# Performance work log

Hardware: AMD Instinct MI355X
Metric: run time of the kernel (lower is better)

## Reference

```python
import jax, jax.numpy as jnp
import numpy as np

N_NODES = 70839  # num_user + num_item from config
N_EDGES = 2_000_000
EMB_DIM = 64
EPS = 1e-12  # torch F.normalize default eps


def setup_inputs() -> dict:
    key = jax.random.key(0)
    k1, k2, k3, k4 = jax.random.split(key, 4)
    ego_embedding = jax.random.normal(k1, (N_NODES, EMB_DIM), dtype=jnp.float32)
    edge_weight = jax.random.uniform(k2, (N_EDGES,), dtype=jnp.float32)
    edge_src = jax.random.randint(k3, (N_EDGES,), 0, N_NODES, dtype=jnp.int32)
    edge_dst = jax.random.randint(k4, (N_EDGES,), 0, N_NODES, dtype=jnp.int32)
    return {
        "ego_embedding": ego_embedding,
        "edge_weight": edge_weight,
        "edge_src": edge_src,
        "edge_dst": edge_dst,
    }


def reference(ego_embedding, edge_weight, edge_src, edge_dst):
    # message: m_e = h[src_e] * w_e   (u_mul_e)
    m = ego_embedding[edge_src] * edge_weight[:, None]          # [E, D]
    # reduce: h_v = sum_{e: dst_e = v} m_e   (fn.sum)
    h = jax.ops.segment_sum(m, edge_dst, num_segments=N_NODES)  # [N, D]
    # F.normalize(h, dim=1, p=2): x / max(||x||_2, eps)
    norm = jnp.linalg.norm(h, axis=1, keepdims=True)
    return h / jnp.maximum(norm, EPS)
```

## Files before the change

kernel.cpp:

```cpp
#include <hip/hip_runtime.h>
#include <hip/hip_fp16.h>

#define EMB_D 64
#define SB 1024
#define SPAN 64
#define SPAN_SH 6
#define MAXG 2048
#define NCHUNK2 512
#define CHMAX 4096
#define TILE2 2048
#define CAST_BLOCKS 256


__device__ __forceinline__ float h15_to_float(unsigned int bits) {
    return __half2float(__ushort_as_half((unsigned short)bits));
}

__device__ __forceinline__ uint4 rowld(const char* base, unsigned int pk,
                                       unsigned int qlo) {
    return *reinterpret_cast<const uint4*>(base + ((pk >> 15) * 128u + qlo));
}

__device__ __forceinline__ void fma8(float4& a, float4& b, uint4 r, float wt) {
    float2 x01 = __half22float2(*reinterpret_cast<__half2*>(&r.x));
    float2 x23 = __half22float2(*reinterpret_cast<__half2*>(&r.y));
    float2 x45 = __half22float2(*reinterpret_cast<__half2*>(&r.z));
    float2 x67 = __half22float2(*reinterpret_cast<__half2*>(&r.w));
    a.x = fmaf(x01.x, wt, a.x); a.y = fmaf(x01.y, wt, a.y);
    a.z = fmaf(x23.x, wt, a.z); a.w = fmaf(x23.y, wt, a.w);
    b.x = fmaf(x45.x, wt, b.x); b.y = fmaf(x45.y, wt, b.y);
    b.z = fmaf(x67.x, wt, b.z); b.w = fmaf(x67.y, wt, b.w);
}

__global__ void a1_cast_hist(const float4* __restrict__ embin,
                             uint2* __restrict__ emb16, int n4,
                             const int* __restrict__ dst,
                             int* __restrict__ cntT,
                             int E, int G, int chunk) {
    if (blockIdx.x < CAST_BLOCKS) {
        int i = blockIdx.x * blockDim.x + threadIdx.x;
        int st = CAST_BLOCKS * blockDim.x;
        for (; i < n4; i += st) {
            float4 v = embin[i];
            __half2 h0 = __float22half2_rn(make_float2(v.x, v.y));
            __half2 h1 = __float22half2_rn(make_float2(v.z, v.w));
            emb16[i] = make_uint2(*reinterpret_cast<unsigned int*>(&h0),
                                  *reinterpret_cast<unsigned int*>(&h1));
        }
    } else {
        __shared__ int bins[MAXG];
        int hb = blockIdx.x - CAST_BLOCKS;
        for (int g = threadIdx.x; g < G; g += blockDim.x) bins[g] = 0;
        __syncthreads();
        int beg = hb * chunk;
        int end = min(beg + chunk, E);
        for (int i = beg + threadIdx.x; i < end; i += blockDim.x)
            atomicAdd(&bins[dst[i] >> SPAN_SH], 1);
        __syncthreads();
        for (int g = threadIdx.x; g < G; g += blockDim.x)
            cntT[g * NCHUNK2 + hb] = bins[g];
    }
}

__global__ void scan_reduceB(const int* __restrict__ counts,
                             int* __restrict__ partial, int M) {
    __shared__ int wsum[16];
    const int tid = threadIdx.x, lane = tid & 63, wid = tid >> 6;
    int i = blockIdx.x * SB + tid;
    int v = (i < M) ? counts[i] : 0;
    #pragma unroll
    for (int off = 32; off > 0; off >>= 1)
        v += __shfl_xor(v, off, 64);
    if (lane == 0) wsum[wid] = v;
    __syncthreads();
    if (tid == 0) {
        int s = 0;
        #pragma unroll
        for (int k = 0; k < 16; ++k) s += wsum[k];
        partial[blockIdx.x] = s;
    }
}

__global__ void scan_apply2(const int* __restrict__ counts,
                            const int* __restrict__ partial,
                            int* __restrict__ offsets, int M, int numB) {
    __shared__ int wsA[16];
    __shared__ int wsB[16];
    __shared__ int wsum[16];
    __shared__ int wpre[16];
    __shared__ int s_boff;
    const int tid = threadIdx.x, lane = tid & 63, wid = tid >> 6;
    const int bid = blockIdx.x;

    int pall = (tid < numB) ? partial[tid] : 0;
    int ppre = (tid < bid) ? pall : 0;
    int sa = pall, sb = ppre;
    #pragma unroll
    for (int off = 32; off > 0; off >>= 1) {
        sa += __shfl_xor(sa, off, 64);
        sb += __shfl_xor(sb, off, 64);
    }
    if (lane == 0) { wsA[wid] = sa; wsB[wid] = sb; }
    __syncthreads();
    if (tid == 0) {
        int a = 0, b = 0;
        #pragma unroll
        for (int k = 0; k < 16; ++k) { a += wsA[k]; b += wsB[k]; }
        s_boff = b;
        if (bid == 0) offsets[M] = a;
    }
    __syncthreads();
    const int boff = s_boff;

    int i = bid * SB + tid;
    int v = (i < M) ? counts[i] : 0;
    int x = v;
    #pragma unroll
    for (int off = 1; off < 64; off <<= 1) {
        int t = __shfl_up(x, off, 64);
        if (lane >= off) x += t;
    }
    if (lane == 63) wsum[wid] = x;
    __syncthreads();
    if (wid == 0) {
        int s = (lane < 16) ? wsum[lane] : 0;
        #pragma unroll
        for (int off = 1; off < 16; off <<= 1) {
            int t = __shfl_up(s, off, 64);
            if (lane >= off) s += t;
        }
        if (lane < 16) wpre[lane] = s;
    }
    __syncthreads();
    int excl = boff + ((wid > 0) ? wpre[wid - 1] : 0) + (x - v);
    if (i < M) offsets[i] = excl;
}

__global__ __launch_bounds__(512) void partition_sort(
        const int* __restrict__ src,
        const int* __restrict__ dst,
        const float* __restrict__ w,
        const int* __restrict__ cntT,
        const int* __restrict__ scanT,
        uint2* __restrict__ stream8,
        int E, int G, int chunk) {
    __shared__ uint2 recs[CHMAX];
    __shared__ int cur[MAXG];
    __shared__ int delta[MAXG];
    __shared__ int wtot[8];

    const int tid = threadIdx.x, lane = tid & 63, wv = tid >> 6;
    const int b = blockIdx.x;
    const int beg = b * chunk;
    const int end = min(beg + chunk, E);
    const int n = end - beg;

    const int K = (G + 511) >> 9;
    int vals[4];
    int acc = 0;
    #pragma unroll
    for (int k = 0; k < 4; ++k) {
        int g = tid * K + k;
        int c = (k < K && g < G) ? cntT[g * NCHUNK2 + b] : 0;
        vals[k] = c;
        acc += c;
    }
    int x = acc;
    #pragma unroll
    for (int off = 1; off < 64; off <<= 1) {
        int t = __shfl_up(x, off, 64);
        if (lane >= off) x += t;
    }
    if (lane == 63) wtot[wv] = x;
    __syncthreads();
    int woff = 0;
    #pragma unroll
    for (int k2 = 0; k2 < 8; ++k2)
        woff += (k2 < wv) ? wtot[k2] : 0;
    int run = woff + x - acc;
    #pragma unroll
    for (int k = 0; k < 4; ++k) {
        int g = tid * K + k;
        if (k < K && g < G) {
            cur[g] = run;
            delta[g] = scanT[g * NCHUNK2 + b] - run;
            run += vals[k];
        }
    }
    __syncthreads();

    for (int i = beg + tid; i < end; i += 512) {
        int d = dst[i];
        unsigned int wb = __half_as_ushort(__float2half_rn(w[i]));
        unsigned int pk = ((unsigned int)src[i] << 15) | (wb & 0x7FFFu);
        int g = d >> SPAN_SH;
        int j = atomicAdd(&cur[g], 1);
        recs[j] = make_uint2(pk, (unsigned int)(d & (SPAN - 1)) |
                                 ((unsigned int)g << SPAN_SH));
    }
    __syncthreads();

    for (int j = tid; j < n; j += 512) {
        uint2 r = recs[j];
        int g = (int)(r.y >> SPAN_SH);
        stream8[delta[g] + j] = make_uint2(r.x, r.y & (SPAN - 1u));
    }
}

__global__ __launch_bounds__(512) void gather_fused64(
        const char* __restrict__ emb16b,
        const uint2* __restrict__ stream8,
        const int* __restrict__ scanT,
        float* __restrict__ out, int N) {
    __shared__ unsigned int srt[TILE2];
    __shared__ int hcnt[SPAN];
    __shared__ int nstart[SPAN];
    __shared__ int cur[SPAN];

    const int g = blockIdx.x;
    const int tid = threadIdx.x;
    const int base = scanT[g * NCHUNK2];
    const int endE = scanT[(g + 1) * NCHUNK2];
    const int crew = tid >> 4;
    const int ql = tid & 15;
    const int sub = ql >> 3;
    const int sl = ql & 7;
    const unsigned qlo = (unsigned)(sl << 4);

    float4 accA[2], accB[2];
    #pragma unroll
    for (int ni = 0; ni < 2; ++ni) {
        accA[ni] = make_float4(0.f, 0.f, 0.f, 0.f);
        accB[ni] = make_float4(0.f, 0.f, 0.f, 0.f);
    }

    for (int tb = base; tb < endE; tb += TILE2) {
        const int n = min(TILE2, endE - tb);
        if (tid < SPAN) hcnt[tid] = 0;
        __syncthreads();
        for (int j = tid; j < n; j += 512)
            atomicAdd(&hcnt[(int)stream8[tb + j].y], 1);
        __syncthreads();
        if (tid < SPAN) {
            int v = hcnt[tid];
            int x = v;
            #pragma unroll
            for (int off = 1; off < 64; off <<= 1) {
                int t = __shfl_up(x, off, 64);
                if (tid >= off) x += t;
            }
            nstart[tid] = x - v;
            cur[tid] = x - v;
        }
        __syncthreads();
        for (int j = tid; j < n; j += 512) {
            uint2 r = stream8[tb + j];
            int slot = atomicAdd(&cur[(int)r.y], 1);
            srt[slot] = r.x;
        }
        __syncthreads();
        #pragma unroll
        for (int ni = 0; ni < 2; ++ni) {
            int nd = crew + (ni << 5);
            int s = nstart[nd];
            int e = cur[nd];
            float4 aA = accA[ni];
            float4 aB = accB[ni];
            int k0 = s + sub;
            unsigned int pk0 = (k0 < e) ? srt[k0] : 0u;
            uint4 r0 = rowld(emb16b, pk0, qlo);
            for (int k = k0; k < e; k += 2) {
                int k1 = k + 2;
                unsigned int pk1 = (k1 < e) ? srt[k1] : 0u;
                uint4 r1 = rowld(emb16b, pk1, qlo);
                fma8(aA, aB, r0, h15_to_float(pk0 & 0x7FFFu));
                pk0 = pk1; r0 = r1;
            }
            accA[ni] = aA;
            accB[ni] = aB;
        }
        __syncthreads();
    }

    #pragma unroll
    for (int ni = 0; ni < 2; ++ni) {
        accA[ni].x += __shfl_xor(accA[ni].x, 8, 64);
        accA[ni].y += __shfl_xor(accA[ni].y, 8, 64);
        accA[ni].z += __shfl_xor(accA[ni].z, 8, 64);
        accA[ni].w += __shfl_xor(accA[ni].w, 8, 64);
        accB[ni].x += __shfl_xor(accB[ni].x, 8, 64);
        accB[ni].y += __shfl_xor(accB[ni].y, 8, 64);
        accB[ni].z += __shfl_xor(accB[ni].z, 8, 64);
        accB[ni].w += __shfl_xor(accB[ni].w, 8, 64);
        int node = g * SPAN + crew + (ni << 5);
        float4 aA = accA[ni];
        float4 aB = accB[ni];
        float ss = aA.x * aA.x + aA.y * aA.y + aA.z * aA.z + aA.w * aA.w
                 + aB.x * aB.x + aB.y * aB.y + aB.z * aB.z + aB.w * aB.w;
        ss += __shfl_xor(ss, 1, 64);
        ss += __shfl_xor(ss, 2, 64);
        ss += __shfl_xor(ss, 4, 64);
        float scale = 1.0f / fmaxf(sqrtf(ss), 1e-12f);
        if (node < N) {
            float4 a = sub ? aB : aA;
            float4 o = make_float4(a.x * scale, a.y * scale,
                                   a.z * scale, a.w * scale);
            *reinterpret_cast<float4*>(out + (size_t)node * EMB_D
                                       + (sl << 3) + (sub << 2)) = o;
        }
    }
}

__global__ void lightgcn_scatter(const float* __restrict__ emb,
                                 const float* __restrict__ w,
                                 const int* __restrict__ src,
                                 const int* __restrict__ dst,
                                 float* __restrict__ h, int E) {
    long long t = (long long)blockIdx.x * blockDim.x + threadIdx.x;
    int e = (int)(t >> 4);
    int d = (int)(t & 15) << 2;
    if (e >= E) return;
    int s = src[e]; int v = dst[e]; float wt = w[e];
    const float4 m = *reinterpret_cast<const float4*>(emb + (size_t)s * EMB_D + d);
    float* o = h + (size_t)v * EMB_D + d;
    unsafeAtomicAdd(o + 0, m.x * wt);
    unsafeAtomicAdd(o + 1, m.y * wt);
    unsafeAtomicAdd(o + 2, m.z * wt);
    unsafeAtomicAdd(o + 3, m.w * wt);
}

__global__ void lightgcn_normalize(float* __restrict__ h, int N) {
    int row = blockIdx.x * (blockDim.x >> 6) + (threadIdx.x >> 6);
    int lane = threadIdx.x & 63;
    if (row >= N) return;
    float x = h[(size_t)row * EMB_D + lane];
    float ss = x * x;
    #pragma unroll
    for (int off = 32; off > 0; off >>= 1)
        ss += __shfl_xor(ss, off, 64);
    h[(size_t)row * EMB_D + lane] = x / fmaxf(sqrtf(ss), 1e-12f);
}

extern "C" void kernel_launch(void* const* d_in, const int* in_sizes, int n_in,
                              void* d_out, int out_size, void* d_ws, size_t ws_size,
                              hipStream_t stream) {
    const float* emb = (const float*)d_in[0];
    const float* w   = (const float*)d_in[1];
    const int*   src = (const int*)d_in[2];
    const int*   dst = (const int*)d_in[3];
    float* out = (float*)d_out;

    const int N = in_sizes[0] / EMB_D;
    const int E = in_sizes[1];
    const int block = 256;
    const int G = (N + SPAN - 1) / SPAN;

    const int M3 = G * NCHUNK2;
    const int numB3 = (M3 + SB - 1) / SB;
    const int chunk3 = (E + NCHUNK2 - 1) / NCHUNK2;

    size_t intsA = (size_t)M3 + (size_t)(M3 + 1) + (size_t)numB3;
    size_t strOff = (intsA * sizeof(int) + 15) & ~(size_t)15;
    size_t embOff = (strOff + (size_t)E * sizeof(uint2) + 15) & ~(size_t)15;
    size_t needed = embOff + (size_t)N * EMB_D * sizeof(__half);

    if (ws_size >= needed && G <= MAXG && chunk3 <= CHMAX && numB3 <= SB &&
        E < (1 << 28) && N < (1 << 17)) {
        int* cntT     = (int*)d_ws;
        int* scanT    = cntT + M3;
        int* partial  = scanT + M3 + 1;
        uint2* stream8 = (uint2*)((char*)d_ws + strOff);
        uint2* emb16 = (uint2*)((char*)d_ws + embOff);

        int n4 = N * (EMB_D / 4);

        a1_cast_hist<<<CAST_BLOCKS + NCHUNK2, block, 0, stream>>>(
            (const float4*)emb, emb16, n4, dst, cntT, E, G, chunk3);

        scan_reduceB<<<numB3, SB, 0, stream>>>(cntT, partial, M3);
        scan_apply2<<<numB3, SB, 0, stream>>>(cntT, partial, scanT, M3, numB3);

        partition_sort<<<NCHUNK2, 512, 0, stream>>>(src, dst, w, cntT, scanT,
                                                    stream8, E, G, chunk3);

        gather_fused64<<<G, 512, 0, stream>>>((const char*)emb16, stream8,
                                              scanT, out, N);
    } else {
        hipMemsetAsync(d_out, 0, (size_t)out_size * sizeof(float), stream);
        long long total = (long long)E * 16;
        int grid = (int)((total + block - 1) / block);
        lightgcn_scatter<<<grid, block, 0, stream>>>(emb, w, src, dst, out, E);
        int gridN = (N + 3) / 4;
        lightgcn_normalize<<<gridN, 256, 0, stream>>>(out, N);
    }
}
```

Before: 187.3 us.

## Replace per-chunk scan with global bucket histogram and atomic cursors, widen bucket span

```diff
diff --git a/kernel.cpp b/kernel.cpp
--- a/kernel.cpp
+++ b/kernel.cpp
@@ -3,13 +3,14 @@
 
 #define EMB_D 64
 #define SB 1024
-#define SPAN 64
-#define SPAN_SH 6
-#define MAXG 2048
+#define SPAN 128
+#define SPAN_SH 7
+#define MAXG 1024
 #define NCHUNK2 512
 #define CHMAX 4096
-#define TILE2 2048
+#define TILE 4096
 #define CAST_BLOCKS 256
+#define HIST_BLOCKS 128
 
 
 __device__ __forceinline__ float h15_to_float(unsigned int bits) {
@@ -32,11 +33,11 @@
     b.z = fmaf(x67.x, wt, b.z); b.w = fmaf(x67.y, wt, b.w);
 }
 
-__global__ void a1_cast_hist(const float4* __restrict__ embin,
+__global__ void f1_cast_hist(const float4* __restrict__ embin,
                              uint2* __restrict__ emb16, int n4,
                              const int* __restrict__ dst,
-                             int* __restrict__ cntT,
-                             int E, int G, int chunk) {
+                             int* __restrict__ hist,
+                             int E, int G, int hchunk) {
     if (blockIdx.x < CAST_BLOCKS) {
         int i = blockIdx.x * blockDim.x + threadIdx.x;
         int st = CAST_BLOCKS * blockDim.x;
@@ -52,68 +53,23 @@
         int hb = blockIdx.x - CAST_BLOCKS;
         for (int g = threadIdx.x; g < G; g += blockDim.x) bins[g] = 0;
         __syncthreads();
-        int beg = hb * chunk;
-        int end = min(beg + chunk, E);
+        int beg = hb * hchunk;
+        int end = min(beg + hchunk, E);
         for (int i = beg + threadIdx.x; i < end; i += blockDim.x)
             atomicAdd(&bins[dst[i] >> SPAN_SH], 1);
         __syncthreads();
         for (int g = threadIdx.x; g < G; g += blockDim.x)
-            cntT[g * NCHUNK2 + hb] = bins[g];
-    }
-}
-
-__global__ void scan_reduceB(const int* __restrict__ counts,
-                             int* __restrict__ partial, int M) {
-    __shared__ int wsum[16];
-    const int tid = threadIdx.x, lane = tid & 63, wid = tid >> 6;
-    int i = blockIdx.x * SB + tid;
-    int v = (i < M) ? counts[i] : 0;
-    #pragma unroll
-    for (int off = 32; off > 0; off >>= 1)
-        v += __shfl_xor(v, off, 64);
-    if (lane == 0) wsum[wid] = v;
-    __syncthreads();
-    if (tid == 0) {
-        int s = 0;
-        #pragma unroll
-        for (int k = 0; k < 16; ++k) s += wsum[k];
-        partial[blockIdx.x] = s;
-    }
-}
-
-__global__ void scan_apply2(const int* __restrict__ counts,
-                            const int* __restrict__ partial,
-                            int* __restrict__ offsets, int M, int numB) {
-    __shared__ int wsA[16];
-    __shared__ int wsB[16];
+            if (bins[g]) atomicAdd(&hist[g], bins[g]);
+    }
+}
+
+__global__ void f2_scan_small(const int* __restrict__ hist,
+                              int* __restrict__ offsets,
+                              int* __restrict__ cursors, int G) {
     __shared__ int wsum[16];
     __shared__ int wpre[16];
-    __shared__ int s_boff;
     const int tid = threadIdx.x, lane = tid & 63, wid = tid >> 6;
-    const int bid = blockIdx.x;
-
-    int pall = (tid < numB) ? partial[tid] : 0;
-    int ppre = (tid < bid) ? pall : 0;
-    int sa = pall, sb = ppre;
-    #pragma unroll
-    for (int off = 32; off > 0; off >>= 1) {
-        sa += __shfl_xor(sa, off, 64);
-        sb += __shfl_xor(sb, off, 64);
-    }
-    if (lane == 0) { wsA[wid] = sa; wsB[wid] = sb; }
-    __syncthreads();
-    if (tid == 0) {
-        int a = 0, b = 0;
-        #pragma unroll
-        for (int k = 0; k < 16; ++k) { a += wsA[k]; b += wsB[k]; }
-        s_boff = b;
-        if (bid == 0) offsets[M] = a;
-    }
-    __syncthreads();
-    const int boff = s_boff;
-
-    int i = bid * SB + tid;
-    int v = (i < M) ? counts[i] : 0;
+    int v = (tid < G) ? hist[tid] : 0;
     int x = v;
     #pragma unroll
     for (int off = 1; off < 64; off <<= 1) {
@@ -132,16 +88,16 @@
         if (lane < 16) wpre[lane] = s;
     }
     __syncthreads();
-    int excl = boff + ((wid > 0) ? wpre[wid - 1] : 0) + (x - v);
-    if (i < M) offsets[i] = excl;
-}
-
-__global__ __launch_bounds__(512) void partition_sort(
+    int excl = ((wid > 0) ? wpre[wid - 1] : 0) + (x - v);
+    if (tid < G) { offsets[tid] = excl; cursors[tid] = excl; }
+    if (tid == 0) offsets[G] = wpre[15];
+}
+
+__global__ __launch_bounds__(512) void partition_atomic(
         const int* __restrict__ src,
         const int* __restrict__ dst,
         const float* __restrict__ w,
-        const int* __restrict__ cntT,
-        const int* __restrict__ scanT,
+        int* __restrict__ cursors,
         uint2* __restrict__ stream8,
         int E, int G, int chunk) {
     __shared__ uint2 recs[CHMAX];
@@ -151,19 +107,26 @@
 
     const int tid = threadIdx.x, lane = tid & 63, wv = tid >> 6;
     const int b = blockIdx.x;
-    const int beg = b * chunk;
+    const int c = (b & 7) * (NCHUNK2 >> 3) + (b >> 3);
+    const int beg = c * chunk;
     const int end = min(beg + chunk, E);
     const int n = end - beg;
 
+    for (int g = tid; g < G; g += 512) cur[g] = 0;
+    __syncthreads();
+    for (int i = beg + tid; i < end; i += 512)
+        atomicAdd(&cur[dst[i] >> SPAN_SH], 1);
+    __syncthreads();
+
     const int K = (G + 511) >> 9;
-    int vals[4];
+    int vals[2];
     int acc = 0;
     #pragma unroll
-    for (int k = 0; k < 4; ++k) {
+    for (int k = 0; k < 2; ++k) {
         int g = tid * K + k;
-        int c = (k < K && g < G) ? cntT[g * NCHUNK2 + b] : 0;
-        vals[k] = c;
-        acc += c;
+        int cc = (k < K && g < G) ? cur[g] : 0;
+        vals[k] = cc;
+        acc += cc;
     }
     int x = acc;
     #pragma unroll
@@ -179,12 +142,14 @@
         woff += (k2 < wv) ? wtot[k2] : 0;
     int run = woff + x - acc;
     #pragma unroll
-    for (int k = 0; k < 4; ++k) {
+    for (int k = 0; k < 2; ++k) {
         int g = tid * K + k;
         if (k < K && g < G) {
+            int cc = vals[k];
             cur[g] = run;
-            delta[g] = scanT[g * NCHUNK2 + b] - run;
-            run += vals[k];
+            if (cc > 0)
+                delta[g] = atomicAdd(&cursors[g], cc) - run;
+            run += cc;
         }
     }
     __syncthreads();
@@ -207,60 +172,69 @@
     }
 }
 
-__global__ __launch_bounds__(512) void gather_fused64(
+__global__ __launch_bounds__(512) void gather_fused(
         const char* __restrict__ emb16b,
         const uint2* __restrict__ stream8,
-        const int* __restrict__ scanT,
+        const int* __restrict__ offsets,
         float* __restrict__ out, int N) {
-    __shared__ unsigned int srt[TILE2];
+    __shared__ uint2 lrec[TILE];
+    __shared__ unsigned int srt[TILE];
     __shared__ int hcnt[SPAN];
     __shared__ int nstart[SPAN];
     __shared__ int cur[SPAN];
+    __shared__ int wtot[2];
 
     const int g = blockIdx.x;
     const int tid = threadIdx.x;
-    const int base = scanT[g * NCHUNK2];
-    const int endE = scanT[(g + 1) * NCHUNK2];
+    const int lane = tid & 63, wv = tid >> 6;
+    const int base = offsets[g];
+    const int endE = offsets[g + 1];
     const int crew = tid >> 4;
     const int ql = tid & 15;
     const int sub = ql >> 3;
     const int sl = ql & 7;
     const unsigned qlo = (unsigned)(sl << 4);
 
-    float4 accA[2], accB[2];
-    #pragma unroll
-    for (int ni = 0; ni < 2; ++ni) {
+    float4 accA[4], accB[4];
+    #pragma unroll
+    for (int ni = 0; ni < 4; ++ni) {
         accA[ni] = make_float4(0.f, 0.f, 0.f, 0.f);
         accB[ni] = make_float4(0.f, 0.f, 0.f, 0.f);
     }
 
-    for (int tb = base; tb < endE; tb += TILE2) {
-        const int n = min(TILE2, endE - tb);
+    for (int tb = base; tb < endE; tb += TILE) {
+        const int n = min(TILE, endE - tb);
         if (tid < SPAN) hcnt[tid] = 0;
-        __syncthreads();
-        for (int j = tid; j < n; j += 512)
-            atomicAdd(&hcnt[(int)stream8[tb + j].y], 1);
-        __syncthreads();
-        if (tid < SPAN) {
-            int v = hcnt[tid];
-            int x = v;
-            #pragma unroll
-            for (int off = 1; off < 64; off <<= 1) {
-                int t = __shfl_up(x, off, 64);
-                if (tid >= off) x += t;
-            }
-            nstart[tid] = x - v;
-            cur[tid] = x - v;
-        }
         __syncthreads();
         for (int j = tid; j < n; j += 512) {
             uint2 r = stream8[tb + j];
-            int slot = atomicAdd(&cur[(int)r.y], 1);
+            lrec[j] = r;
+            atomicAdd(&hcnt[r.y], 1);
+        }
+        __syncthreads();
+        int v = (tid < SPAN) ? hcnt[tid] : 0;
+        int x = v;
+        #pragma unroll
+        for (int off = 1; off < 64; off <<= 1) {
+            int t = __shfl_up(x, off, 64);
+            if (lane >= off) x += t;
+        }
+        if (wv < 2 && lane == 63) wtot[wv] = x;
+        __syncthreads();
+        if (tid < SPAN) {
+            int excl = x - v + ((wv == 1) ? wtot[0] : 0);
+            nstart[tid] = excl;
+            cur[tid] = excl;
+        }
+        __syncthreads();
+        for (int j = tid; j < n; j += 512) {
+            uint2 r = lrec[j];
+            int slot = atomicAdd(&cur[r.y], 1);
             srt[slot] = r.x;
         }
         __syncthreads();
         #pragma unroll
-        for (int ni = 0; ni < 2; ++ni) {
+        for (int ni = 0; ni < 4; ++ni) {
             int nd = crew + (ni << 5);
             int s = nstart[nd];
             int e = cur[nd];
@@ -283,7 +257,7 @@
     }
 
     #pragma unroll
-    for (int ni = 0; ni < 2; ++ni) {
+    for (int ni = 0; ni < 4; ++ni) {
         accA[ni].x += __shfl_xor(accA[ni].x, 8, 64);
         accA[ni].y += __shfl_xor(accA[ni].y, 8, 64);
         accA[ni].z += __shfl_xor(accA[ni].z, 8, 64);
@@ -354,37 +328,36 @@
     const int E = in_sizes[1];
     const int block = 256;
     const int G = (N + SPAN - 1) / SPAN;
-
-    const int M3 = G * NCHUNK2;
-    const int numB3 = (M3 + SB - 1) / SB;
-    const int chunk3 = (E + NCHUNK2 - 1) / NCHUNK2;
-
-    size_t intsA = (size_t)M3 + (size_t)(M3 + 1) + (size_t)numB3;
-    size_t strOff = (intsA * sizeof(int) + 15) & ~(size_t)15;
+    const int chunk = (E + NCHUNK2 - 1) / NCHUNK2;
+    const int hchunk = (E + HIST_BLOCKS - 1) / HIST_BLOCKS;
+
+    size_t ints = 3 * (size_t)G + 1;
+    size_t strOff = (ints * sizeof(int) + 15) & ~(size_t)15;
     size_t embOff = (strOff + (size_t)E * sizeof(uint2) + 15) & ~(size_t)15;
     size_t needed = embOff + (size_t)N * EMB_D * sizeof(__half);
 
-    if (ws_size >= needed && G <= MAXG && chunk3 <= CHMAX && numB3 <= SB &&
+    if (ws_size >= needed && G <= MAXG && chunk <= CHMAX &&
         E < (1 << 28) && N < (1 << 17)) {
-        int* cntT     = (int*)d_ws;
-        int* scanT    = cntT + M3;
-        int* partial  = scanT + M3 + 1;
+        int* hist    = (int*)d_ws;
+        int* offsets = hist + G;
+        int* cursors = offsets + G + 1;
         uint2* stream8 = (uint2*)((char*)d_ws + strOff);
         uint2* emb16 = (uint2*)((char*)d_ws + embOff);
 
         int n4 = N * (EMB_D / 4);
 
-        a1_cast_hist<<<CAST_BLOCKS + NCHUNK2, block, 0, stream>>>(
-            (const float4*)emb, emb16, n4, dst, cntT, E, G, chunk3);
-
-        scan_reduceB<<<numB3, SB, 0, stream>>>(cntT, partial, M3);
-        scan_apply2<<<numB3, SB, 0, stream>>>(cntT, partial, scanT, M3, numB3);
-
-        partition_sort<<<NCHUNK2, 512, 0, stream>>>(src, dst, w, cntT, scanT,
-                                                    stream8, E, G, chunk3);
-
-        gather_fused64<<<G, 512, 0, stream>>>((const char*)emb16, stream8,
-                                              scanT, out, N);
+        hipMemsetAsync(hist, 0, (size_t)G * sizeof(int), stream);
+
+        f1_cast_hist<<<CAST_BLOCKS + HIST_BLOCKS, block, 0, stream>>>(
+            (const float4*)emb, emb16, n4, dst, hist, E, G, hchunk);
+
+        f2_scan_small<<<1, SB, 0, stream>>>(hist, offsets, cursors, G);
+
+        partition_atomic<<<NCHUNK2, 512, 0, stream>>>(src, dst, w, cursors,
+                                                      stream8, E, G, chunk);
+
+        gather_fused<<<G, 512, 0, stream>>>((const char*)emb16, stream8,
+                                            offsets, out, N);
     } else {
         hipMemsetAsync(d_out, 0, (size_t)out_size * sizeof(float), stream);
         long long total = (long long)E * 16;
```

Measured after the change: 182.5 us. -2.5%, faster.
